# Kernel tuning notes

Hardware: AMD Instinct MI355X
Metric: run time of the kernel (lower is better)

Reference implementation:

```python
import jax, jax.numpy as jnp
import numpy as np

TOP_K = 2
NUM_EXPERTS = 8
ROUTE_SCALE = 1.0


def setup_inputs() -> dict:
    key = jax.random.key(0)
    ks = jax.random.split(key, 8)
    bs, slen, dim, hidden, E = 4, 1024, 2048, 1024, NUM_EXPERTS
    s = 0.02
    return {
        "x": jax.random.normal(ks[0], (bs, slen, dim), jnp.float32),
        "gate_w": jax.random.normal(ks[1], (E, dim), jnp.float32) * s,
        "w1": jax.random.normal(ks[2], (E, hidden, dim), jnp.float32) * s,
        "w2": jax.random.normal(ks[3], (E, dim, hidden), jnp.float32) * s,
        "w3": jax.random.normal(ks[4], (E, hidden, dim), jnp.float32) * s,
        "ws1": jax.random.normal(ks[5], (hidden, dim), jnp.float32) * s,
        "ws2": jax.random.normal(ks[6], (dim, hidden), jnp.float32) * s,
        "ws3": jax.random.normal(ks[7], (hidden, dim), jnp.float32) * s,
    }


def reference(x, gate_w, w1, w2, w3, ws1, ws2, ws3):
    bs, slen, dim = x.shape
    xf = x.reshape(-1, dim)  # (T, dim)
    # --- router: sigmoid scores in fp32, top-k (expert_bias is zeros at init) ---
    logits = (xf @ gate_w.T).astype(jnp.float32)  # (T, E)
    scores = jax.nn.sigmoid(logits)
    top_scores, sel_idx = jax.lax.top_k(scores, TOP_K)  # (T, k), (T, k)
    top_scores = top_scores * ROUTE_SCALE  # route_norm=False
    # --- routed experts: score_before_experts=True -> scale input by score ---
    routed = jnp.zeros_like(xf)
    for k in range(TOP_K):
        xs = xf * top_scores[:, k][:, None]  # (T, dim)
        h1 = jnp.einsum('td,ehd->teh', xs, w1)
        h3 = jnp.einsum('td,ehd->teh', xs, w3)
        h = jax.nn.silu(h1) * h3  # (T, E, hidden)
        onehot = jax.nn.one_hot(sel_idx[:, k], NUM_EXPERTS, dtype=h.dtype)  # (T, E)
        routed = routed + jnp.einsum('teh,te,edh->td', h, onehot, w2)
    # --- shared expert (SwiGLU FFN) ---
    shared = (jax.nn.silu(xf @ ws1.T) * (xf @ ws3.T)) @ ws2.T
    out = (shared + routed).reshape(bs, slen, dim)
    return out
```

## Files before the change

### kernel.cpp

```cpp
#include <hip/hip_runtime.h>
#include <hip/hip_bf16.h>
#include <cstdint>

#define TTOK   4096
#define DIM    2048
#define HID    1024
#define NEXP   8
#define GROWS  12288

typedef __attribute__((ext_vector_type(8))) __bf16 bf16x8;
typedef __attribute__((ext_vector_type(4))) float  f32x4;

__device__ __forceinline__ void glds16(const void* g, void* l) {
  __builtin_amdgcn_global_load_lds((const __attribute__((address_space(1))) void*)g,
                                   (__attribute__((address_space(3))) void*)l,
                                   16, 0, 0);
}

#define BAR() do { asm volatile("" ::: "memory"); __builtin_amdgcn_s_barrier(); \
                   asm volatile("" ::: "memory"); } while (0)

__global__ void convert_router_k(const float* __restrict__ w1, const float* __restrict__ w2,
                                 const float* __restrict__ w3, const float* __restrict__ ws1,
                                 const float* __restrict__ ws2, const float* __restrict__ ws3,
                                 __bf16* __restrict__ w13, __bf16* __restrict__ w2c,
                                 const float* __restrict__ x, const float* __restrict__ gw,
                                 int* __restrict__ sel, float* __restrict__ sco,
                                 int* __restrict__ counts) {
  const int N1 = 9 * 2048 * 2048 / 8;
  const int N2 = 9 * 2048 * 1024 / 8;
  const int CONV_BLOCKS = (N1 + N2) / 256;

  if (blockIdx.x < (unsigned)CONV_BLOCKS) {
    int s = blockIdx.x * 256 + threadIdx.x;
    const float* src;
    __bf16* dst;
    if (s < N1) {
      int e  = s / 524288;
      int r  = (s % 524288) / 256;
      int c  = (s % 256) * 8;
      int nr;
      if (r < 1024) { src = (e < 8 ? w1 + ((size_t)e * 1024 + r) * 2048 : ws1 + (size_t)r * 2048) + c;
                      nr = 2 * r; }
      else          { src = (e < 8 ? w3 + ((size_t)e * 1024 + (r - 1024)) * 2048 : ws3 + (size_t)(r - 1024) * 2048) + c;
                      nr = 2 * (r - 1024) + 1; }
      dst = w13 + ((size_t)e * 2048 + nr) * 2048 + c;
    } else {
      int s2 = s - N1;
      int e  = s2 / 262144;
      int r  = (s2 % 262144) / 128;
      int c  = (s2 % 128) * 8;
      src = (e < 8 ? w2 + ((size_t)e * 2048 + r) * 1024 : ws2 + (size_t)r * 1024) + c;
      dst = w2c + ((size_t)e * 2048 + r) * 1024 + c;
    }
    float4 a = *(const float4*)(src);
    float4 b = *(const float4*)(src + 4);
    bf16x8 o;
    o[0]=(__bf16)a.x; o[1]=(__bf16)a.y; o[2]=(__bf16)a.z; o[3]=(__bf16)a.w;
    o[4]=(__bf16)b.x; o[5]=(__bf16)b.y; o[6]=(__bf16)b.z; o[7]=(__bf16)b.w;
    *(bf16x8*)dst = o;
    return;
  }

  int t    = (blockIdx.x - CONV_BLOCKS) * 4 + (threadIdx.x >> 6);
  int lane = threadIdx.x & 63;
  const float* xr = x + (size_t)t * DIM;
  float acc[NEXP];
  #pragma unroll
  for (int e = 0; e < NEXP; ++e) acc[e] = 0.f;
  for (int d = lane * 4; d < DIM; d += 256) {
    float4 xv = *(const float4*)(xr + d);
    #pragma unroll
    for (int e = 0; e < NEXP; ++e) {
      float4 gv = *(const float4*)(gw + (size_t)e * DIM + d);
      acc[e] += xv.x * gv.x + xv.y * gv.y + xv.z * gv.z + xv.w * gv.w;
    }
  }
  #pragma unroll
  for (int off = 32; off; off >>= 1)
    #pragma unroll
    for (int e = 0; e < NEXP; ++e) acc[e] += __shfl_xor(acc[e], off);
  if (lane == 0) {
    float s[NEXP];
    #pragma unroll
    for (int e = 0; e < NEXP; ++e) s[e] = 1.f / (1.f + expf(-acc[e]));
    int e0 = 0;
    #pragma unroll
    for (int e = 1; e < NEXP; ++e) if (s[e] > s[e0]) e0 = e;
    int e1 = (e0 == 0) ? 1 : 0;
    #pragma unroll
    for (int e = 0; e < NEXP; ++e) if (e != e0 && s[e] > s[e1]) e1 = e;
    sel[2 * t] = e0; sel[2 * t + 1] = e1;
    sco[2 * t] = s[e0]; sco[2 * t + 1] = s[e1];
    atomicAdd(&counts[e0], 1); atomicAdd(&counts[e1], 1);
  }
}

__global__ void scan_k(const int* __restrict__ counts, int* __restrict__ offs) {
  if (threadIdx.x == 0 && blockIdx.x == 0) {
    int o = 0;
    for (int e = 0; e < NEXP; ++e) { offs[e] = o; o += counts[e]; }
    offs[NEXP] = o;
    offs[NEXP + 1] = o + TTOK;
  }
}

__global__ void gather_k(const float* __restrict__ x, const int* __restrict__ sel,
                         const float* __restrict__ sco, const int* __restrict__ offs,
                         int* __restrict__ cursor, int* __restrict__ token_rows,
                         __bf16* __restrict__ xg) {
  __shared__ int   rows[3];
  __shared__ float ss[3];
  int t = blockIdx.x;
  if (threadIdx.x == 0) {
    int e0 = sel[2 * t], e1 = sel[2 * t + 1];
    int r0 = offs[e0] + atomicAdd(&cursor[e0], 1);
    int r1 = offs[e1] + atomicAdd(&cursor[e1], 1);
    int r2 = 8192 + t;
    rows[0] = r0; rows[1] = r1; rows[2] = r2;
    ss[0] = sco[2 * t]; ss[1] = sco[2 * t + 1]; ss[2] = 1.0f;
    token_rows[3 * t] = r0; token_rows[3 * t + 1] = r1; token_rows[3 * t + 2] = r2;
  }
  __syncthreads();
  int c = threadIdx.x * 8;
  float4 v0 = *(const float4*)(x + (size_t)t * DIM + c);
  float4 v1 = *(const float4*)(x + (size_t)t * DIM + c + 4);
  #pragma unroll
  for (int j = 0; j < 3; ++j) {
    float s = ss[j];
    bf16x8 o;
    o[0]=(__bf16)(v0.x*s); o[1]=(__bf16)(v0.y*s); o[2]=(__bf16)(v0.z*s); o[3]=(__bf16)(v0.w*s);
    o[4]=(__bf16)(v1.x*s); o[5]=(__bf16)(v1.y*s); o[6]=(__bf16)(v1.z*s); o[7]=(__bf16)(v1.w*s);
    *(bf16x8*)(xg + (size_t)rows[j] * DIM + c) = o;
  }
}

template <int EPI>
__launch_bounds__(256)
__global__ void gemm_nt(const __bf16* __restrict__ A, const __bf16* __restrict__ Bw,
                        __bf16* __restrict__ Hb, float* __restrict__ c2a, float* __restrict__ c2b,
                        const int* __restrict__ offs, int K_, int N_) {
  int z  = blockIdx.z;
  int o0 = offs[z];
  int ne = offs[z + 1] - o0;

  int flat = blockIdx.y * 32 + blockIdx.x;
  int nid  = (flat & 7) * 64 + (flat >> 3);
  int bm   = nid & 31;
  int bn   = nid >> 5;

  if (bm * 128 >= ne) return;

  const __bf16* Aseg = A  + (size_t)(o0 + bm * 128) * K_;
  const __bf16* Bseg = Bw + ((size_t)z * N_ + bn * 128) * K_;

  __shared__ __align__(16) __bf16 sA[2][128 * 64];
  __shared__ __align__(16) __bf16 sB[2][128 * 64];

  int tid  = threadIdx.x;
  int wave = tid >> 6, lane = tid & 63;
  int wm = wave & 1, wn = wave >> 1;
  int fr = lane & 15;
  int fq = lane >> 4;
  int sw = fr & 7;

  f32x4 acc[4][4];
  #pragma unroll
  for (int i = 0; i < 4; ++i)
    #pragma unroll
    for (int j = 0; j < 4; ++j) acc[i][j] = (f32x4){0.f, 0.f, 0.f, 0.f};

#define STAGE(buf, kbase)                                                     \
  {                                                                           \
    _Pragma("unroll")                                                         \
    for (int it = 0; it < 4; ++it) {                                          \
      int s   = it * 256 + tid;                                               \
      int row = s >> 3;                                                       \
      int c8  = (s & 7) ^ (row & 7);                                          \
      glds16(Aseg + (size_t)row * K_ + (kbase) + c8 * 8, &sA[buf][s * 8]);    \
      glds16(Bseg + (size_t)row * K_ + (kbase) + c8 * 8, &sB[buf][s * 8]);    \
    }                                                                         \
  }

  STAGE(0, 0)
  asm volatile("s_waitcnt vmcnt(0)" ::: "memory");
  BAR();

  const int nk = K_ >> 6;
  for (int t = 0; t < nk; ++t) {
    int cur = t & 1;
    if (t + 1 < nk) {
      STAGE(cur ^ 1, (t + 1) << 6)
      asm volatile("s_waitcnt vmcnt(8)" ::: "memory");
    } else {
      asm volatile("s_waitcnt vmcnt(0)" ::: "memory");
    }
    BAR();

    const __bf16* rAbase = &sA[cur][(wm * 64 + fr) * 64];
    const __bf16* rBbase = &sB[cur][(wn * 64 + fr) * 64];
    #pragma unroll
    for (int kk = 0; kk < 2; ++kk) {
      int slot = ((kk * 4 + fq) ^ sw) * 8;
      bf16x8 af[4], bb[4];
      #pragma unroll
      for (int i = 0; i < 4; ++i) af[i] = *(const bf16x8*)(rAbase + i * 16 * 64 + slot);
      #pragma unroll
      for (int i = 0; i < 4; ++i) bb[i] = *(const bf16x8*)(rBbase + i * 16 * 64 + slot);
      #pragma unroll
      for (int mi = 0; mi < 4; ++mi)
        #pragma unroll
        for (int ni = 0; ni < 4; ++ni)
          acc[mi][ni] = __builtin_amdgcn_mfma_f32_16x16x32_bf16(af[mi], bb[ni], acc[mi][ni], 0, 0, 0);
    }
    BAR();
  }
#undef STAGE

  #pragma unroll
  for (int mi = 0; mi < 4; ++mi) {
    #pragma unroll
    for (int r = 0; r < 4; ++r) {
      int rl = bm * 128 + wm * 64 + mi * 16 + fq * 4 + r;
      bool ok = rl < ne;
      int grow = o0 + rl;
      if (EPI == 0) {
        #pragma unroll
        for (int ni = 0; ni < 4; ++ni) {
          float v = acc[mi][ni][r];
          float o = __shfl_xor(v, 1);
          float h1 = (fr & 1) ? o : v;
          float h3 = (fr & 1) ? v : o;
          float g  = h1 / (1.f + expf(-h1)) * h3;
          if (ok && !(fr & 1)) {
            int hcol = bn * 64 + wn * 32 + ni * 8 + (fr >> 1);
            Hb[(size_t)grow * 1024 + hcol] = (__bf16)g;
          }
        }
      } else {
        if (ok) {
          float* dst = (grow < 8192) ? (c2a + (size_t)grow * 2048)
                                     : (c2b + (size_t)(grow - 8192) * 2048);
          #pragma unroll
          for (int ni = 0; ni < 4; ++ni) {
            int col = bn * 128 + wn * 64 + ni * 16 + fr;
            dst[col] = acc[mi][ni][r];
          }
        }
      }
    }
  }
}

__global__ void combine_k(const float* __restrict__ c2a, const float* __restrict__ c2b,
                          const int* __restrict__ token_rows, float* __restrict__ out) {
  __shared__ int rr[3];
  int t = blockIdx.x;
  if (threadIdx.x < 3) rr[threadIdx.x] = token_rows[3 * t + threadIdx.x];
  __syncthreads();
  int c = threadIdx.x * 8;
  const float* p0 = c2a + (size_t)rr[0] * 2048 + c;
  const float* p1 = c2a + (size_t)rr[1] * 2048 + c;
  const float* p2 = c2b + (size_t)(rr[2] - 8192) * 2048 + c;
  float4 a0 = *(const float4*)p0,       a1 = *(const float4*)p1,       a2 = *(const float4*)p2;
  float4 b0 = *(const float4*)(p0 + 4), b1 = *(const float4*)(p1 + 4), b2 = *(const float4*)(p2 + 4);
  float4 oa, ob;
  oa.x = a0.x + a1.x + a2.x; oa.y = a0.y + a1.y + a2.y;
  oa.z = a0.z + a1.z + a2.z; oa.w = a0.w + a1.w + a2.w;
  ob.x = b0.x + b1.x + b2.x; ob.y = b0.y + b1.y + b2.y;
  ob.z = b0.z + b1.z + b2.z; ob.w = b0.w + b1.w + b2.w;
  float* op = out + (size_t)t * 2048 + c;
  *(float4*)op = oa;
  *(float4*)(op + 4) = ob;
}

extern "C" void kernel_launch(void* const* d_in, const int* in_sizes, int n_in,
                              void* d_out, int out_size, void* d_ws, size_t ws_size,
                              hipStream_t stream) {
  const float* x   = (const float*)d_in[0];
  const float* gw  = (const float*)d_in[1];
  const float* w1  = (const float*)d_in[2];
  const float* w2  = (const float*)d_in[3];
  const float* w3  = (const float*)d_in[4];
  const float* ws1 = (const float*)d_in[5];
  const float* ws2 = (const float*)d_in[6];
  const float* ws3 = (const float*)d_in[7];
  float* out = (float*)d_out;

  char* p = (char*)d_ws;
  int*   counts     = (int*)p;
  int*   cursor     = (int*)(p + 64);
  int*   offs       = (int*)(p + 128);
  int*   sel        = (int*)(p + 1024);
  float* sco        = (float*)(p + 1024 + 32768);
  int*   token_rows = (int*)(p + 1024 + 65536);
  char* big = p + (1 << 20);
  __bf16* w13  = (__bf16*)big;
  __bf16* w2c  = (__bf16*)(big + 75497472ull);
  __bf16* xg   = (__bf16*)(big + 75497472ull + 37748736ull);
  __bf16* hbuf = (__bf16*)(big + 75497472ull + 37748736ull + 50331648ull);
  float*  c2a  = (float*)w13;
  float*  c2b  = (float*)xg;

  hipMemsetAsync(p, 0, 256, stream);

  convert_router_k<<<27648 + TTOK / 4, 256, 0, stream>>>(w1, w2, w3, ws1, ws2, ws3, w13, w2c,
                                                         x, gw, sel, sco, counts);
  scan_k<<<1, 64, 0, stream>>>(counts, offs);
  gather_k<<<TTOK, 256, 0, stream>>>(x, sel, sco, offs, cursor, token_rows, xg);
  gemm_nt<0><<<dim3(32, 16, 9), 256, 0, stream>>>(xg, w13, hbuf, nullptr, nullptr, offs, 2048, 2048);
  gemm_nt<1><<<dim3(32, 16, 9), 256, 0, stream>>>(hbuf, w2c, nullptr, c2a, c2b, offs, 1024, 2048);
  combine_k<<<TTOK, 256, 0, stream>>>(c2a, c2b, token_rows, out);
}
```

Before: 743.4 us.

## Split convert/router kernels, fuse scan into router, rework both expert GEMMs

Weight conversion and routing become separate kernels, and the prefix scan now runs in the last router block, found through an atomic done counter. The first GEMM becomes a 128-thread kernel with two waves, each computing a 64x128 tile held in a 4x8 accumulator array, using single-buffered LDS with plain __syncthreads. The second GEMM unrolls its double buffering into explicitly named buffers with COMPUTE/STAGE macros. The aim is to cut a launch and raise per-wave MFMA work, but the single-buffered GEMM loses its load/compute overlap and uses more registers.

```diff
diff --git a/kernel.cpp b/kernel.cpp
--- a/kernel.cpp
+++ b/kernel.cpp
@@ -17,52 +17,47 @@
                                    16, 0, 0);
 }
 
-#define BAR() do { asm volatile("" ::: "memory"); __builtin_amdgcn_s_barrier(); \
-                   asm volatile("" ::: "memory"); } while (0)
-
-__global__ void convert_router_k(const float* __restrict__ w1, const float* __restrict__ w2,
-                                 const float* __restrict__ w3, const float* __restrict__ ws1,
-                                 const float* __restrict__ ws2, const float* __restrict__ ws3,
-                                 __bf16* __restrict__ w13, __bf16* __restrict__ w2c,
-                                 const float* __restrict__ x, const float* __restrict__ gw,
-                                 int* __restrict__ sel, float* __restrict__ sco,
-                                 int* __restrict__ counts) {
+__global__ void convert_w(const float* __restrict__ w1, const float* __restrict__ w2,
+                          const float* __restrict__ w3, const float* __restrict__ ws1,
+                          const float* __restrict__ ws2, const float* __restrict__ ws3,
+                          __bf16* __restrict__ w13, __bf16* __restrict__ w2c) {
   const int N1 = 9 * 2048 * 2048 / 8;
   const int N2 = 9 * 2048 * 1024 / 8;
-  const int CONV_BLOCKS = (N1 + N2) / 256;
-
-  if (blockIdx.x < (unsigned)CONV_BLOCKS) {
-    int s = blockIdx.x * 256 + threadIdx.x;
-    const float* src;
-    __bf16* dst;
-    if (s < N1) {
-      int e  = s / 524288;
-      int r  = (s % 524288) / 256;
-      int c  = (s % 256) * 8;
-      int nr;
-      if (r < 1024) { src = (e < 8 ? w1 + ((size_t)e * 1024 + r) * 2048 : ws1 + (size_t)r * 2048) + c;
-                      nr = 2 * r; }
-      else          { src = (e < 8 ? w3 + ((size_t)e * 1024 + (r - 1024)) * 2048 : ws3 + (size_t)(r - 1024) * 2048) + c;
-                      nr = 2 * (r - 1024) + 1; }
-      dst = w13 + ((size_t)e * 2048 + nr) * 2048 + c;
-    } else {
-      int s2 = s - N1;
-      int e  = s2 / 262144;
-      int r  = (s2 % 262144) / 128;
-      int c  = (s2 % 128) * 8;
-      src = (e < 8 ? w2 + ((size_t)e * 2048 + r) * 1024 : ws2 + (size_t)r * 1024) + c;
-      dst = w2c + ((size_t)e * 2048 + r) * 1024 + c;
-    }
-    float4 a = *(const float4*)(src);
-    float4 b = *(const float4*)(src + 4);
-    bf16x8 o;
-    o[0]=(__bf16)a.x; o[1]=(__bf16)a.y; o[2]=(__bf16)a.z; o[3]=(__bf16)a.w;
-    o[4]=(__bf16)b.x; o[5]=(__bf16)b.y; o[6]=(__bf16)b.z; o[7]=(__bf16)b.w;
-    *(bf16x8*)dst = o;
-    return;
-  }
-
-  int t    = (blockIdx.x - CONV_BLOCKS) * 4 + (threadIdx.x >> 6);
+  int s = blockIdx.x * 256 + threadIdx.x;
+  const float* src;
+  __bf16* dst;
+  if (s < N1) {
+    int e  = s / 524288;
+    int r  = (s % 524288) / 256;
+    int c  = (s % 256) * 8;
+    int nr;
+    if (r < 1024) { src = (e < 8 ? w1 + ((size_t)e * 1024 + r) * 2048 : ws1 + (size_t)r * 2048) + c;
+                    nr = 2 * r; }
+    else          { src = (e < 8 ? w3 + ((size_t)e * 1024 + (r - 1024)) * 2048 : ws3 + (size_t)(r - 1024) * 2048) + c;
+                    nr = 2 * (r - 1024) + 1; }
+    dst = w13 + ((size_t)e * 2048 + nr) * 2048 + c;
+  } else {
+    int s2 = s - N1;
+    if (s2 >= N2) return;
+    int e  = s2 / 262144;
+    int r  = (s2 % 262144) / 128;
+    int c  = (s2 % 128) * 8;
+    src = (e < 8 ? w2 + ((size_t)e * 2048 + r) * 1024 : ws2 + (size_t)r * 1024) + c;
+    dst = w2c + ((size_t)e * 2048 + r) * 1024 + c;
+  }
+  float4 a = *(const float4*)(src);
+  float4 b = *(const float4*)(src + 4);
+  bf16x8 o;
+  o[0]=(__bf16)a.x; o[1]=(__bf16)a.y; o[2]=(__bf16)a.z; o[3]=(__bf16)a.w;
+  o[4]=(__bf16)b.x; o[5]=(__bf16)b.y; o[6]=(__bf16)b.z; o[7]=(__bf16)b.w;
+  *(bf16x8*)dst = o;
+}
+
+__global__ void router_k(const float* __restrict__ x, const float* __restrict__ gw,
+                         int* __restrict__ sel, float* __restrict__ sco,
+                         int* __restrict__ counts, int* __restrict__ done,
+                         int* __restrict__ offs) {
+  int t    = blockIdx.x * 4 + (threadIdx.x >> 6);
   int lane = threadIdx.x & 63;
   const float* xr = x + (size_t)t * DIM;
   float acc[NEXP];
@@ -94,14 +89,20 @@
     sco[2 * t] = s[e0]; sco[2 * t + 1] = s[e1];
     atomicAdd(&counts[e0], 1); atomicAdd(&counts[e1], 1);
   }
-}
-
-__global__ void scan_k(const int* __restrict__ counts, int* __restrict__ offs) {
-  if (threadIdx.x == 0 && blockIdx.x == 0) {
-    int o = 0;
-    for (int e = 0; e < NEXP; ++e) { offs[e] = o; o += counts[e]; }
-    offs[NEXP] = o;
-    offs[NEXP + 1] = o + TTOK;
+  __syncthreads();
+  if (threadIdx.x == 0) {
+    __threadfence();
+    int old = atomicAdd(done, 1);
+    if (old == gridDim.x - 1) {
+      int o = 0;
+      #pragma unroll
+      for (int e = 0; e < NEXP; ++e) {
+        int c = atomicAdd(&counts[e], 0);
+        offs[e] = o; o += c;
+      }
+      offs[NEXP] = o;
+      offs[NEXP + 1] = o + TTOK;
+    }
   }
 }
 
@@ -135,11 +136,10 @@
   }
 }
 
-template <int EPI>
-__launch_bounds__(256)
-__global__ void gemm_nt(const __bf16* __restrict__ A, const __bf16* __restrict__ Bw,
-                        __bf16* __restrict__ Hb, float* __restrict__ c2a, float* __restrict__ c2b,
-                        const int* __restrict__ offs, int K_, int N_) {
+__launch_bounds__(128)
+__global__ void gemm_wide(const __bf16* __restrict__ A, const __bf16* __restrict__ Bw,
+                          __bf16* __restrict__ Hb, const int* __restrict__ offs,
+                          int K_, int N_) {
   int z  = blockIdx.z;
   int o0 = offs[z];
   int ne = offs[z + 1] - o0;
@@ -154,8 +154,102 @@
   const __bf16* Aseg = A  + (size_t)(o0 + bm * 128) * K_;
   const __bf16* Bseg = Bw + ((size_t)z * N_ + bn * 128) * K_;
 
-  __shared__ __align__(16) __bf16 sA[2][128 * 64];
-  __shared__ __align__(16) __bf16 sB[2][128 * 64];
+  __shared__ __align__(16) __bf16 sA[128 * 64];
+  __shared__ __align__(16) __bf16 sB[128 * 64];
+
+  int tid  = threadIdx.x;
+  int wave = tid >> 6, lane = tid & 63;
+  int fr = lane & 15;
+  int fq = lane >> 4;
+  int sw = fr & 7;
+
+  int rA0 = tid >> 3;
+  int c8  = (tid & 7) ^ (rA0 & 7);
+  const __bf16* aP = Aseg + (size_t)rA0 * K_ + c8 * 8;
+  const __bf16* bP = Bseg + (size_t)rA0 * K_ + c8 * 8;
+
+  f32x4 acc[4][8];
+  #pragma unroll
+  for (int i = 0; i < 4; ++i)
+    #pragma unroll
+    for (int j = 0; j < 8; ++j) acc[i][j] = (f32x4){0.f, 0.f, 0.f, 0.f};
+
+  const int nk = K_ >> 6;
+  for (int t = 0; t < nk; ++t) {
+    int k0 = t << 6;
+    #pragma unroll
+    for (int it = 0; it < 8; ++it) {
+      glds16(aP + k0 + (size_t)it * 16 * K_, &sA[(it * 128 + tid) * 8]);
+      glds16(bP + k0 + (size_t)it * 16 * K_, &sB[(it * 128 + tid) * 8]);
+    }
+    __syncthreads();
+    #pragma unroll
+    for (int kk = 0; kk < 2; ++kk) {
+      int slot = ((kk * 4 + fq) ^ sw) * 8;
+      bf16x8 af[4], bb[8];
+      #pragma unroll
+      for (int i = 0; i < 4; ++i)
+        af[i] = *(const bf16x8*)(sA + (wave * 64 + i * 16 + fr) * 64 + slot);
+      #pragma unroll
+      for (int j = 0; j < 8; ++j)
+        bb[j] = *(const bf16x8*)(sB + (j * 16 + fr) * 64 + slot);
+      #pragma unroll
+      for (int i = 0; i < 4; ++i)
+        #pragma unroll
+        for (int j = 0; j < 8; ++j)
+          acc[i][j] = __builtin_amdgcn_mfma_f32_16x16x32_bf16(af[i], bb[j], acc[i][j], 0, 0, 0);
+    }
+    __syncthreads();
+  }
+
+  #pragma unroll
+  for (int mi = 0; mi < 4; ++mi) {
+    #pragma unroll
+    for (int r = 0; r < 4; ++r) {
+      int rl = bm * 128 + wave * 64 + mi * 16 + fq * 4 + r;
+      bool ok = rl < ne;
+      int grow = o0 + rl;
+      #pragma unroll
+      for (int ni = 0; ni < 8; ++ni) {
+        float v = acc[mi][ni][r];
+        float o = __shfl_xor(v, 1);
+        float h1 = (fr & 1) ? o : v;
+        float h3 = (fr & 1) ? v : o;
+        float g  = h1 / (1.f + expf(-h1)) * h3;
+        if (ok && !(fr & 1)) {
+          int hcol = bn * 64 + ni * 8 + (fr >> 1);
+          Hb[(size_t)grow * 1024 + hcol] = (__bf16)g;
+        }
+      }
+    }
+  }
+}
+
+#define BAR() do { asm volatile("" ::: "memory"); __builtin_amdgcn_s_barrier(); \
+                   asm volatile("" ::: "memory"); } while (0)
+
+__launch_bounds__(256)
+__global__ void gemm_nt2(const __bf16* __restrict__ A, const __bf16* __restrict__ Bw,
+                         float* __restrict__ c2a, float* __restrict__ c2b,
+                         const int* __restrict__ offs, int K_, int N_) {
+  int z  = blockIdx.z;
+  int o0 = offs[z];
+  int ne = offs[z + 1] - o0;
+
+  int flat = blockIdx.y * 32 + blockIdx.x;
+  int nid  = (flat & 7) * 64 + (flat >> 3);
+  int bm   = nid & 31;
+  int bn   = nid >> 5;
+
+  if (bm * 128 >= ne) return;
+
+  const __bf16* Aseg = A  + (size_t)(o0 + bm * 128) * K_;
+  const __bf16* Bseg = Bw + ((size_t)z * N_ + bn * 128) * K_;
+
+  __shared__ __align__(16) __bf16 sA0[128 * 64];
+  __shared__ __align__(16) __bf16 sB0[128 * 64];
+  __shared__ __align__(16) __bf16 sA1[128 * 64];
+  __shared__ __align__(16) __bf16 sB1[128 * 64];
 
   int tid  = threadIdx.x;
   int wave = tid >> 6, lane = tid & 63;
@@ -170,82 +264,81 @@
     #pragma unroll
     for (int j = 0; j < 4; ++j) acc[i][j] = (f32x4){0.f, 0.f, 0.f, 0.f};
 
-#define STAGE(buf, kbase)                                                     \
+#define STAGE(dA, dB, kbase)                                                  \
   {                                                                           \
     _Pragma("unroll")                                                         \
     for (int it = 0; it < 4; ++it) {                                          \
       int s   = it * 256 + tid;                                               \
       int row = s >> 3;                                                       \
-      int c8  = (s & 7) ^ (row & 7);                                          \
-      glds16(Aseg + (size_t)row * K_ + (kbase) + c8 * 8, &sA[buf][s * 8]);    \
-      glds16(Bseg + (size_t)row * K_ + (kbase) + c8 * 8, &sB[buf][s * 8]);    \
+      int cc  = (s & 7) ^ (row & 7);                                          \
+      glds16(Aseg + (size_t)row * K_ + (kbase) + cc * 8, &dA[s * 8]);         \
+      glds16(Bseg + (size_t)row * K_ + (kbase) + cc * 8, &dB[s * 8]);         \
     }                                                                         \
   }
 
-  STAGE(0, 0)
+#define COMPUTE(pA, pB)                                                       \
+  {                                                                           \
+    const __bf16* rAbase = pA + (wm * 64 + fr) * 64;                          \
+    const __bf16* rBbase = pB + (wn * 64 + fr) * 64;                          \
+    _Pragma("unroll")                                                         \
+    for (int kk = 0; kk < 2; ++kk) {                                          \
+      int slot = ((kk * 4 + fq) ^ sw) * 8;                                    \
+      bf16x8 af[4], bb[4];                                                    \
+      _Pragma("unroll")                                                       \
+      for (int i = 0; i < 4; ++i) af[i] = *(const bf16x8*)(rAbase + i * 16 * 64 + slot); \
+      _Pragma("unroll")                                                       \
+      for (int i = 0; i < 4; ++i) bb[i] = *(const bf16x8*)(rBbase + i * 16 * 64 + slot); \
+      _Pragma("unroll")                                                       \
+      for (int mi = 0; mi < 4; ++mi)                                          \
+        _Pragma("unroll")                                                     \
+        for (int ni = 0; ni < 4; ++ni)                                        \
+          acc[mi][ni] = __builtin_amdgcn_mfma_f32_16x16x32_bf16(af[mi], bb[ni], acc[mi][ni], 0, 0, 0); \
+    }                                                                         \
+  }
+
+  STAGE(sA0, sB0, 0)
   asm volatile("s_waitcnt vmcnt(0)" ::: "memory");
   BAR();
 
   const int nk = K_ >> 6;
-  for (int t = 0; t < nk; ++t) {
-    int cur = t & 1;
+  for (int t = 0; t < nk; t += 2) {
     if (t + 1 < nk) {
-      STAGE(cur ^ 1, (t + 1) << 6)
+      STAGE(sA1, sB1, (t + 1) << 6)
       asm volatile("s_waitcnt vmcnt(8)" ::: "memory");
     } else {
       asm volatile("s_waitcnt vmcnt(0)" ::: "memory");
     }
     BAR();
-
-    const __bf16* rAbase = &sA[cur][(wm * 64 + fr) * 64];
-    const __bf16* rBbase = &sB[cur][(wn * 64 + fr) * 64];
-    #pragma unroll
-    for (int kk = 0; kk < 2; ++kk) {
-      int slot = ((kk * 4 + fq) ^ sw) * 8;
-      bf16x8 af[4], bb[4];
-      #pragma unroll
-      for (int i = 0; i < 4; ++i) af[i] = *(const bf16x8*)(rAbase + i * 16 * 64 + slot);
-      #pragma unroll
-      for (int i = 0; i < 4; ++i) bb[i] = *(const bf16x8*)(rBbase + i * 16 * 64 + slot);
-      #pragma unroll
-      for (int mi = 0; mi < 4; ++mi)
-        #pragma unroll
-        for (int ni = 0; ni < 4; ++ni)
-          acc[mi][ni] = __builtin_amdgcn_mfma_f32_16x16x32_bf16(af[mi], bb[ni], acc[mi][ni], 0, 0, 0);
-    }
+    COMPUTE(sA0, sB0)
     BAR();
+    if (t + 1 < nk) {
+      if (t + 2 < nk) {
+        STAGE(sA0, sB0, (t + 2) << 6)
+        asm volatile("s_waitcnt vmcnt(8)" ::: "memory");
+      } else {
+        asm volatile("s_waitcnt vmcnt(0)" ::: "memory");
+      }
+      BAR();
+      COMPUTE(sA1, sB1)
+      BAR();
+    }
   }
 #undef STAGE
+#undef COMPUTE
 
   #pragma unroll
   for (int mi = 0; mi < 4; ++mi) {
     #pragma unroll
     for (int r = 0; r < 4; ++r) {
       int rl = bm * 128 + wm * 64 + mi * 16 + fq * 4 + r;
-      bool ok = rl < ne;
-      int grow = o0 + rl;
-      if (EPI == 0) {
+      if (rl < ne) {
+        int grow = o0 + rl;
+        float* dst = (grow < 8192) ? (c2a + (size_t)grow * 2048)
+                                   : (c2b + (size_t)(grow - 8192) * 2048);
         #pragma unroll
         for (int ni = 0; ni < 4; ++ni) {
-          float v = acc[mi][ni][r];
-          float o = __shfl_xor(v, 1);
-          float h1 = (fr & 1) ? o : v;
-          float h3 = (fr & 1) ? v : o;
-          float g  = h1 / (1.f + expf(-h1)) * h3;
-          if (ok && !(fr & 1)) {
-            int hcol = bn * 64 + wn * 32 + ni * 8 + (fr >> 1);
-            Hb[(size_t)grow * 1024 + hcol] = (__bf16)g;
-          }
-        }
-      } else {
-        if (ok) {
-          float* dst = (grow < 8192) ? (c2a + (size_t)grow * 2048)
-                                     : (c2b + (size_t)(grow - 8192) * 2048);
-          #pragma unroll
-          for (int ni = 0; ni < 4; ++ni) {
-            int col = bn * 128 + wn * 64 + ni * 16 + fr;
-            dst[col] = acc[mi][ni][r];
-          }
+          int col = bn * 128 + wn * 64 + ni * 16 + fr;
+          dst[col] = acc[mi][ni][r];
         }
       }
     }
@@ -291,6 +384,7 @@
   int*   counts     = (int*)p;
   int*   cursor     = (int*)(p + 64);
   int*   offs       = (int*)(p + 128);
+  int*   done       = (int*)(p + 192);
   int*   sel        = (int*)(p + 1024);
   float* sco        = (float*)(p + 1024 + 32768);
   int*   token_rows = (int*)(p + 1024 + 65536);
@@ -304,11 +398,10 @@
 
   hipMemsetAsync(p, 0, 256, stream);
 
-  convert_router_k<<<27648 + TTOK / 4, 256, 0, stream>>>(w1, w2, w3, ws1, ws2, ws3, w13, w2c,
-                                                         x, gw, sel, sco, counts);
-  scan_k<<<1, 64, 0, stream>>>(counts, offs);
+  convert_w<<<27648, 256, 0, stream>>>(w1, w2, w3, ws1, ws2, ws3, w13, w2c);
+  router_k<<<TTOK / 4, 256, 0, stream>>>(x, gw, sel, sco, counts, done, offs);
   gather_k<<<TTOK, 256, 0, stream>>>(x, sel, sco, offs, cursor, token_rows, xg);
-  gemm_nt<0><<<dim3(32, 16, 9), 256, 0, stream>>>(xg, w13, hbuf, nullptr, nullptr, offs, 2048, 2048);
-  gemm_nt<1><<<dim3(32, 16, 9), 256, 0, stream>>>(hbuf, w2c, nullptr, c2a, c2b, offs, 1024, 2048);
+  gemm_wide<<<dim3(32, 16, 9), 128, 0, stream>>>(xg, w13, hbuf, offs, 2048, 2048);
+  gemm_nt2<<<dim3(32, 16, 9), 256, 0, stream>>>(hbuf, w2c, c2a, c2b, offs, 1024, 2048);
   combine_k<<<TTOK, 256, 0, stream>>>(c2a, c2b, token_rows, out);
 }
```

Result: slower. 823.9 us (+10.8%).
